# Kernel tuning notes

Hardware: AMD Instinct MI355X
Metric: run time of the kernel (lower is better)

Reference implementation:

```python
import jax, jax.numpy as jnp
import numpy as np

CH, G, K, STRIDE, RR = 256, 16, 7, 1, 4
GROUP = CH // G            # channels per group
PAD = (K - 1) // 2
BN_EPS = 1e-5


def setup_inputs() -> dict:
    key = jax.random.key(0)
    ks = jax.random.split(key, 9)
    b, dim = 16, 4096
    hid = CH // RR  # 64
    return {
        "x": jax.random.normal(ks[0], (b, CH, dim), jnp.float32),
        "w1": jax.random.normal(ks[1], (hid, CH), jnp.float32) * (1.0 / np.sqrt(CH)),
        "b1": jax.random.normal(ks[2], (hid,), jnp.float32) * 0.02,
        "bn_gamma": 1.0 + 0.1 * jax.random.normal(ks[3], (hid,), jnp.float32),
        "bn_beta": 0.1 * jax.random.normal(ks[4], (hid,), jnp.float32),
        "bn_mean": 0.1 * jax.random.normal(ks[5], (hid,), jnp.float32),
        "bn_var": jax.random.uniform(ks[6], (hid,), jnp.float32) + 0.5,
        "w2": jax.random.normal(ks[7], (K * G, hid), jnp.float32) * (1.0 / np.sqrt(hid)),
        "b2": jax.random.normal(ks[8], (K * G,), jnp.float32) * 0.02,
    }


def _involution(x, w1, b1, bn_gamma, bn_beta, bn_mean, bn_var, w2, b2):
    b, ch, dim = x.shape
    L = dim // STRIDE  # out_dim
    # unfold: pad then gather K shifted strided views -> [b, ch, K, L]
    xp = jnp.pad(x, ((0, 0), (0, 0), (PAD, PAD)))
    unfolded = jnp.stack(
        [xp[:, :, k : k + STRIDE * (L - 1) + 1 : STRIDE] for k in range(K)], axis=2
    )
    unfolded = unfolded.reshape(b, G, GROUP, K, L)
    # adaptive max pool to L (windows of size STRIDE); identity when STRIDE == 1
    pooled = x.reshape(b, ch, L, STRIDE).max(axis=-1)
    # kernel generator: 1x1 conv -> relu -> batchnorm (inference) -> 1x1 conv
    h = jnp.einsum("oc,bcl->bol", w1, pooled) + b1[:, None]
    h = jax.nn.relu(h)
    h = (h - bn_mean[:, None]) * jax.lax.rsqrt(bn_var[:, None] + BN_EPS)
    h = h * bn_gamma[:, None] + bn_beta[:, None]
    kern = jnp.einsum("oc,bcl->bol", w2, h) + b2[:, None]  # [b, K*G, L]
    kern = kern.reshape(b, G, K, L)
    # per-location dynamic kernel multiply + reduce over K
    out = jnp.einsum("bgkl,bgckl->bgcl", kern, unfolded)
    return out.reshape(b, ch, L)


def reference(x, w1, b1, bn_gamma, bn_beta, bn_mean, bn_var, w2, b2):
    return _involution(x, w1, b1, bn_gamma, bn_beta, bn_mean, bn_var, w2, b2)
```

## Files before the change

### kernel.cpp

```cpp
#include <hip/hip_runtime.h>

#define BB   16
#define CHN  256
#define DIMN 4096
#define KK   7
#define HID  64
#define KGN  112
#define TLC  32
#define XSD  19
#define XSH  38
#define HSTH 38
#define KSTD 36
#define BN_EPS 1e-5f

typedef __fp16 half2_t __attribute__((ext_vector_type(2)));
typedef __fp16 half8   __attribute__((ext_vector_type(8)));
typedef float  f32x4   __attribute__((ext_vector_type(4)));

union U32H2 { unsigned int u; half2_t h; };

static __device__ __forceinline__ unsigned int packf(float a, float b) {
    U32H2 t; t.h = __builtin_amdgcn_cvt_pkrtz(a, b); return t.u;
}
static __device__ __forceinline__ half2_t ash2(unsigned int u) { U32H2 t; t.u = u; return t.h; }
static __device__ __forceinline__ __fp16 u16h(unsigned short u) {
    return __builtin_bit_cast(__fp16, u);
}
static __device__ __forceinline__ unsigned short hu16(__fp16 h) {
    return __builtin_bit_cast(unsigned short, h);
}

static __device__ __forceinline__ void bar_lds() {
    asm volatile("s_waitcnt lgkmcnt(0)" ::: "memory");
    __builtin_amdgcn_s_barrier();
    __builtin_amdgcn_sched_barrier(0);
}

__global__ __launch_bounds__(256) void setup_k(
    const float* __restrict__ w1, const float* __restrict__ w2,
    const float* __restrict__ bn_gamma, const float* __restrict__ bn_beta,
    const float* __restrict__ bn_mean,  const float* __restrict__ bn_var,
    __fp16* __restrict__ w1f, __fp16* __restrict__ w2f,
    float* __restrict__ scb, float* __restrict__ shb) {
    int t = blockIdx.x * 256 + threadIdx.x;
    if (t < HID * CHN) w1f[t] = (__fp16)w1[t];
    if (t < KGN * HID) w2f[t] = (__fp16)w2[t];
    if (t < HID) {
        float s = bn_gamma[t] * rsqrtf(bn_var[t] + BN_EPS);
        scb[t] = s;
        shb[t] = bn_beta[t] - bn_mean[t] * s;
    }
}

template <int OFF>
static __device__ __forceinline__ void extract_kv(const uint4 q[4], float kv[KK][4]) {
#pragma unroll
    for (int k = 0; k < KK; ++k) {
        const int kk = k + OFF;
        const int i  = kk >> 1;
        const int h  = kk & 1;
#pragma unroll
        for (int j = 0; j < 4; ++j) {
            unsigned int u = (&q[i].x)[j];
            half2_t hh = ash2(u);
            kv[k][j] = h ? (float)hh[1] : (float)hh[0];
        }
    }
}

__global__ __launch_bounds__(256, 5) void fused_k(
    const float* __restrict__ x,
    const __fp16* __restrict__ w1f,
    const float* __restrict__ b1,
    const float* __restrict__ scb, const float* __restrict__ shb,
    const __fp16* __restrict__ w2f,
    const float* __restrict__ b2,
    float* __restrict__ out) {
    __shared__ unsigned int xs[CHN * XSD];
    __shared__ unsigned int un[56 * KSTD];

    unsigned short* xs16 = (unsigned short*)xs;
    unsigned short* hs16 = (unsigned short*)un;
    unsigned int*   ks   = un;

    const int t    = threadIdx.x;
    const int lane = t & 63;
    const int w    = t >> 6;
    const int lr   = t & 15;
    const int lg   = (t >> 4) & 3;

    const int L  = (blockIdx.x & 7) * 256 + (blockIdx.x >> 3);
    const int b  = L >> 7;
    const int l0 = (L & 127) * TLC;

    {
        const int colq = t & 7;
        const int chl  = t >> 3;
        const float* xg = x + ((size_t)b * CHN + chl) * DIMN + l0 + 4 * colq;
        float4 v[8];
#pragma unroll
        for (int i = 0; i < 8; ++i)
            v[i] = *(const float4*)(xg + (size_t)(32 * i) * DIMN);
#pragma unroll
        for (int i = 0; i < 8; ++i) {
            unsigned short* rp = xs16 + (chl + 32 * i) * XSH + 4 * colq + 3;
            rp[0] = hu16((__fp16)v[i].x);
            *(unsigned int*)(rp + 1) = packf(v[i].y, v[i].z);
            rp[3] = hu16((__fp16)v[i].w);
        }
        const float* xrow = x + ((size_t)b * CHN + t) * DIMN;
        unsigned short* hp = xs16 + t * XSH;
#pragma unroll
        for (int j = 0; j < 3; ++j) {
            int dl = l0 - 3 + j;
            float lvv = (dl >= 0) ? xrow[dl] : 0.0f;
            hp[j] = hu16((__fp16)lvv);
            int dr = l0 + TLC + j;
            float rvv = (dr < DIMN) ? xrow[dr] : 0.0f;
            hp[35 + j] = hu16((__fp16)rvv);
        }
    }
    bar_lds();

    f32x4 acc[2];
#pragma unroll
    for (int cf = 0; cf < 2; ++cf) acc[cf] = (f32x4){0.f, 0.f, 0.f, 0.f};

#pragma unroll
    for (int p = 0; p < 8; ++p) {
        half8 af = *(const half8*)(w1f + (16 * w + lr) * CHN + 32 * p + 8 * lg);
#pragma unroll
        for (int cf = 0; cf < 2; ++cf) {
            half8 bf;
#pragma unroll
            for (int j = 0; j < 8; ++j)
                bf[j] = u16h(xs16[(32 * p + 8 * lg + j) * XSH + 16 * cf + lr + 3]);
            acc[cf] = __builtin_amdgcn_mfma_f32_16x16x32_f16(af, bf, acc[cf], 0, 0, 0);
        }
    }

#pragma unroll
    for (int cf = 0; cf < 2; ++cf) {
#pragma unroll
        for (int r = 0; r < 4; ++r) {
            const int o = 16 * w + 4 * lg + r;
            float hv = fmaxf(acc[cf][r] + b1[o], 0.f) * scb[o] + shb[o];
            hs16[o * HSTH + 16 * cf + lr] = hu16((__fp16)hv);
        }
    }
    bar_lds();

    const int nrf = (w < 3) ? 2 : 1;
    f32x4 acc2[2][2];
#pragma unroll
    for (int ri = 0; ri < 2; ++ri)
#pragma unroll
        for (int cf = 0; cf < 2; ++cf) acc2[ri][cf] = (f32x4){0.f, 0.f, 0.f, 0.f};

#pragma unroll
    for (int kx = 0; kx < 2; ++kx) {
        half8 bf[2];
#pragma unroll
        for (int cf = 0; cf < 2; ++cf)
#pragma unroll
            for (int j = 0; j < 8; ++j)
                bf[cf][j] = u16h(hs16[(32 * kx + 8 * lg + j) * HSTH + 16 * cf + lr]);
        for (int ri = 0; ri < nrf; ++ri) {
            const int rf = w + 4 * ri;
            half8 af = *(const half8*)(w2f + (16 * rf + lr) * HID + 32 * kx + 8 * lg);
            acc2[ri][0] = __builtin_amdgcn_mfma_f32_16x16x32_f16(af, bf[0], acc2[ri][0], 0, 0, 0);
            acc2[ri][1] = __builtin_amdgcn_mfma_f32_16x16x32_f16(af, bf[1], acc2[ri][1], 0, 0, 0);
        }
    }
    bar_lds();

    for (int ri = 0; ri < nrf; ++ri) {
        const int rf = w + 4 * ri;
#pragma unroll
        for (int cf = 0; cf < 2; ++cf) {
#pragma unroll
            for (int p2 = 0; p2 < 2; ++p2) {
                const int r0 = 16 * rf + 4 * lg + 2 * p2;
                float k0 = acc2[ri][cf][2 * p2 + 0] + b2[r0 + 0];
                float k1 = acc2[ri][cf][2 * p2 + 1] + b2[r0 + 1];
                ks[(r0 >> 1) * KSTD + 16 * cf + lr] = packf(k0, k1);
            }
        }
    }
    bar_lds();

    const int q4    = lane & 7;
    const int hi    = lane >> 3;
    const int cbase = 4 * q4;

#pragma unroll
    for (int gi = 0; gi < 4; ++gi) {
        const int g   = 4 * w + gi;
        const int rpb = (7 * g) >> 1;
        uint4 qq[4];
#pragma unroll
        for (int ii = 0; ii < 4; ++ii)
            qq[ii] = *(const uint4*)(ks + (rpb + ii) * KSTD + cbase);
        float kv[KK][4];
        if ((gi & 1) == 0) extract_kv<0>(qq, kv);
        else               extract_kv<1>(qq, kv);

#pragma unroll
        for (int i2 = 0; i2 < 2; ++i2) {
            const int ch = 16 * g + 8 * i2 + hi;
            const unsigned int* xr = xs + ch * XSD + (cbase >> 1);
            unsigned int uu[5];
#pragma unroll
            for (int j = 0; j < 5; ++j) uu[j] = xr[j];
            float xv[10];
#pragma unroll
            for (int r = 0; r < 10; ++r) {
                half2_t hh = ash2(uu[r >> 1]);
                xv[r] = (r & 1) ? (float)hh[1] : (float)hh[0];
            }
            float o0 = 0.f, o1 = 0.f, o2 = 0.f, o3 = 0.f;
#pragma unroll
            for (int k = 0; k < KK; ++k) {
                o0 = fmaf(kv[k][0], xv[k + 0], o0);
                o1 = fmaf(kv[k][1], xv[k + 1], o1);
                o2 = fmaf(kv[k][2], xv[k + 2], o2);
                o3 = fmaf(kv[k][3], xv[k + 3], o3);
            }
            *(float4*)(out + ((size_t)b * CHN + ch) * DIMN + l0 + cbase) =
                make_float4(o0, o1, o2, o3);
        }
    }
}

extern "C" void kernel_launch(void* const* d_in, const int* in_sizes, int n_in,
                              void* d_out, int out_size, void* d_ws, size_t ws_size,
                              hipStream_t stream) {
    (void)in_sizes; (void)n_in; (void)out_size; (void)ws_size;

    const float* x        = (const float*)d_in[0];
    const float* w1       = (const float*)d_in[1];
    const float* b1       = (const float*)d_in[2];
    const float* bn_gamma = (const float*)d_in[3];
    const float* bn_beta  = (const float*)d_in[4];
    const float* bn_mean  = (const float*)d_in[5];
    const float* bn_var   = (const float*)d_in[6];
    const float* w2       = (const float*)d_in[7];
    const float* b2       = (const float*)d_in[8];
    float*       out      = (float*)d_out;

    __fp16* w1f = (__fp16*)d_ws;
    __fp16* w2f = w1f + HID * CHN;
    float*  scb = (float*)(w2f + KGN * HID);
    float*  shb = scb + HID;

    setup_k<<<(HID * CHN + 255) / 256, 256, 0, stream>>>(
        w1, w2, bn_gamma, bn_beta, bn_mean, bn_var, w1f, w2f, scb, shb);
    fused_k<<<BB * (DIMN / TLC), 256, 0, stream>>>(
        x, w1f, b1, scb, shb, w2f, b2, out);
}
```

Baseline: 55.06 us.

## Transpose x tile in LDS with swizzle and reload x from global for involution

Stores the x tile in LDS transposed (column-major, channels contiguous) with an XOR swizzle, so the first GEMM's B fragments load as single 16-byte vectors instead of eight scalar halfword reads. The hidden tile is stored transposed as well, enabling vector B loads for the second GEMM, and one barrier is removed because the kernel-weight buffer no longer aliases the hidden buffer. The final involution step now rereads x from global memory (likely L2-resident) in fp32 with halo handling instead of reading LDS. This adds strided 4-byte global loads during staging and extra global traffic in the epilogue, but improves precision and cuts LDS instructions.

```diff
diff --git a/kernel.cpp b/kernel.cpp
--- a/kernel.cpp
+++ b/kernel.cpp
@@ -7,9 +7,8 @@
 #define HID  64
 #define KGN  112
 #define TLC  32
-#define XSD  19
-#define XSH  38
-#define HSTH 38
+#define XKS  132
+#define HTS  33
 #define KSTD 36
 #define BN_EPS 1e-5f
 
@@ -23,12 +22,6 @@
     U32H2 t; t.h = __builtin_amdgcn_cvt_pkrtz(a, b); return t.u;
 }
 static __device__ __forceinline__ half2_t ash2(unsigned int u) { U32H2 t; t.u = u; return t.h; }
-static __device__ __forceinline__ __fp16 u16h(unsigned short u) {
-    return __builtin_bit_cast(__fp16, u);
-}
-static __device__ __forceinline__ unsigned short hu16(__fp16 h) {
-    return __builtin_bit_cast(unsigned short, h);
-}
 
 static __device__ __forceinline__ void bar_lds() {
     asm volatile("s_waitcnt lgkmcnt(0)" ::: "memory");
@@ -76,12 +69,12 @@
     const __fp16* __restrict__ w2f,
     const float* __restrict__ b2,
     float* __restrict__ out) {
-    __shared__ unsigned int xs[CHN * XSD];
-    __shared__ unsigned int un[56 * KSTD];
-
-    unsigned short* xs16 = (unsigned short*)xs;
-    unsigned short* hs16 = (unsigned short*)un;
-    unsigned int*   ks   = un;
+    __shared__ unsigned int xkt[TLC * XKS];
+    __shared__ unsigned int hst[TLC * HTS];
+    __shared__ unsigned int ks[56 * KSTD];
+
+    const unsigned short* xkt16 = (const unsigned short*)xkt;
+    const unsigned short* hst16 = (const unsigned short*)hst;
 
     const int t    = threadIdx.x;
     const int lane = t & 63;
@@ -94,30 +87,21 @@
     const int l0 = (L & 127) * TLC;
 
     {
-        const int colq = t & 7;
-        const int chl  = t >> 3;
-        const float* xg = x + ((size_t)b * CHN + chl) * DIMN + l0 + 4 * colq;
-        float4 v[8];
-#pragma unroll
-        for (int i = 0; i < 8; ++i)
-            v[i] = *(const float4*)(xg + (size_t)(32 * i) * DIMN);
+        const int col = t & 31;
+        const int chq = t >> 5;
+        const int xsw = (col & 7) << 4;
+        const float* xg = x + (size_t)b * CHN * DIMN + l0 + col;
 #pragma unroll
         for (int i = 0; i < 8; ++i) {
-            unsigned short* rp = xs16 + (chl + 32 * i) * XSH + 4 * colq + 3;
-            rp[0] = hu16((__fp16)v[i].x);
-            *(unsigned int*)(rp + 1) = packf(v[i].y, v[i].z);
-            rp[3] = hu16((__fp16)v[i].w);
-        }
-        const float* xrow = x + ((size_t)b * CHN + t) * DIMN;
-        unsigned short* hp = xs16 + t * XSH;
-#pragma unroll
-        for (int j = 0; j < 3; ++j) {
-            int dl = l0 - 3 + j;
-            float lvv = (dl >= 0) ? xrow[dl] : 0.0f;
-            hp[j] = hu16((__fp16)lvv);
-            int dr = l0 + TLC + j;
-            float rvv = (dr < DIMN) ? xrow[dr] : 0.0f;
-            hp[35 + j] = hu16((__fp16)rvv);
+            const int ch0 = 4 * chq + 32 * i;
+            float f0 = xg[(size_t)(ch0 + 0) * DIMN];
+            float f1 = xg[(size_t)(ch0 + 1) * DIMN];
+            float f2 = xg[(size_t)(ch0 + 2) * DIMN];
+            float f3 = xg[(size_t)(ch0 + 3) * DIMN];
+            uint2 u;
+            u.x = packf(f0, f1);
+            u.y = packf(f2, f3);
+            *(uint2*)&xkt[col * XKS + (((ch0 >> 1)) ^ xsw)] = u;
         }
     }
     bar_lds();
@@ -131,22 +115,26 @@
         half8 af = *(const half8*)(w1f + (16 * w + lr) * CHN + 32 * p + 8 * lg);
 #pragma unroll
         for (int cf = 0; cf < 2; ++cf) {
-            half8 bf;
-#pragma unroll
-            for (int j = 0; j < 8; ++j)
-                bf[j] = u16h(xs16[(32 * p + 8 * lg + j) * XSH + 16 * cf + lr + 3]);
+            const int col = 16 * cf + lr;
+            const int dwo = col * XKS + ((16 * p + 4 * lg) ^ ((col & 7) << 4));
+            half8 bf = *(const half8*)(xkt16 + 2 * dwo);
             acc[cf] = __builtin_amdgcn_mfma_f32_16x16x32_f16(af, bf, acc[cf], 0, 0, 0);
         }
     }
 
 #pragma unroll
     for (int cf = 0; cf < 2; ++cf) {
+        const int col = 16 * cf + lr;
+        float hv[4];
 #pragma unroll
         for (int r = 0; r < 4; ++r) {
             const int o = 16 * w + 4 * lg + r;
-            float hv = fmaxf(acc[cf][r] + b1[o], 0.f) * scb[o] + shb[o];
-            hs16[o * HSTH + 16 * cf + lr] = hu16((__fp16)hv);
-        }
+            hv[r] = fmaxf(acc[cf][r] + b1[o], 0.f) * scb[o] + shb[o];
+        }
+        uint2 u;
+        u.x = packf(hv[0], hv[1]);
+        u.y = packf(hv[2], hv[3]);
+        *(uint2*)&hst[col * HTS + 8 * w + 2 * lg] = u;
     }
     bar_lds();
 
@@ -161,10 +149,10 @@
     for (int kx = 0; kx < 2; ++kx) {
         half8 bf[2];
 #pragma unroll
-        for (int cf = 0; cf < 2; ++cf)
-#pragma unroll
-            for (int j = 0; j < 8; ++j)
-                bf[cf][j] = u16h(hs16[(32 * kx + 8 * lg + j) * HSTH + 16 * cf + lr]);
+        for (int cf = 0; cf < 2; ++cf) {
+            const int col = 16 * cf + lr;
+            bf[cf] = *(const half8*)(hst16 + 2 * (col * HTS + 16 * kx + 4 * lg));
+        }
         for (int ri = 0; ri < nrf; ++ri) {
             const int rf = w + 4 * ri;
             half8 af = *(const half8*)(w2f + (16 * rf + lr) * HID + 32 * kx + 8 * lg);
@@ -172,7 +160,6 @@
             acc2[ri][1] = __builtin_amdgcn_mfma_f32_16x16x32_f16(af, bf[1], acc2[ri][1], 0, 0, 0);
         }
     }
-    bar_lds();
 
     for (int ri = 0; ri < nrf; ++ri) {
         const int rf = w + 4 * ri;
@@ -192,6 +179,7 @@
     const int q4    = lane & 7;
     const int hi    = lane >> 3;
     const int cbase = 4 * q4;
+    const int col0  = l0 + cbase;
 
 #pragma unroll
     for (int gi = 0; gi < 4; ++gi) {
@@ -208,25 +196,24 @@
 #pragma unroll
         for (int i2 = 0; i2 < 2; ++i2) {
             const int ch = 16 * g + 8 * i2 + hi;
-            const unsigned int* xr = xs + ch * XSD + (cbase >> 1);
-            unsigned int uu[5];
-#pragma unroll
-            for (int j = 0; j < 5; ++j) uu[j] = xr[j];
-            float xv[10];
-#pragma unroll
-            for (int r = 0; r < 10; ++r) {
-                half2_t hh = ash2(uu[r >> 1]);
-                xv[r] = (r & 1) ? (float)hh[1] : (float)hh[0];
+            const float* xrow = x + ((size_t)b * CHN + ch) * DIMN;
+            float4 fa = *(const float4*)(xrow + (col0 > 0 ? col0 - 4 : 0));
+            float4 fb = *(const float4*)(xrow + col0);
+            float4 fc = *(const float4*)(xrow + (col0 + 4 < DIMN ? col0 + 4 : DIMN - 4));
+
+            float xr[10] = { fa.y, fa.z, fa.w, fb.x, fb.y, fb.z, fb.w, fc.x, fc.y, fc.z };
+            if (col0 == 0)        { xr[0] = 0.f; xr[1] = 0.f; xr[2] = 0.f; }
+            if (col0 == DIMN - 4) { xr[7] = 0.f; xr[8] = 0.f; xr[9] = 0.f; }
+
+            float o0 = 0.f, o1 = 0.f, o2 = 0.f, o3 = 0.f;
+#pragma unroll
+            for (int k = 0; k < KK; ++k) {
+                o0 = fmaf(kv[k][0], xr[k + 0], o0);
+                o1 = fmaf(kv[k][1], xr[k + 1], o1);
+                o2 = fmaf(kv[k][2], xr[k + 2], o2);
+                o3 = fmaf(kv[k][3], xr[k + 3], o3);
             }
-            float o0 = 0.f, o1 = 0.f, o2 = 0.f, o3 = 0.f;
-#pragma unroll
-            for (int k = 0; k < KK; ++k) {
-                o0 = fmaf(kv[k][0], xv[k + 0], o0);
-                o1 = fmaf(kv[k][1], xv[k + 1], o1);
-                o2 = fmaf(kv[k][2], xv[k + 2], o2);
-                o3 = fmaf(kv[k][3], xv[k + 3], o3);
-            }
-            *(float4*)(out + ((size_t)b * CHN + ch) * DIMN + l0 + cbase) =
+            *(float4*)(out + ((size_t)b * CHN + ch) * DIMN + col0) =
                 make_float4(o0, o1, o2, o3);
         }
     }
```

Result: faster. 51.20 us, median of 2 (-7.0%).
